# Kernel optimization log

Hardware: AMD Instinct MI355X
Metric: run time of the kernel (lower is better)

Reference implementation:

```python
import jax, jax.numpy as jnp
import numpy as np

EMBED_DIM = 512
NUM_HEADS = 8
HEAD_DIM = EMBED_DIM // NUM_HEADS
B, N, M = 4, 4096, 4096


def setup_inputs() -> dict:
    key = jax.random.key(0)
    ks = jax.random.split(key, 16)
    s = 0.02
    inp = {
        "query": jax.random.normal(ks[0], (B, N, EMBED_DIM), jnp.float32),
        "key": jax.random.normal(ks[1], (B, M, EMBED_DIM), jnp.float32),
        "value": jax.random.normal(ks[2], (B, M, EMBED_DIM), jnp.float32),
        # Linear weights stored as (in, out) so y = x @ W + b (== torch x @ W.T + b)
        "Wq": jax.random.normal(ks[3], (EMBED_DIM, EMBED_DIM), jnp.float32) * s,
        "bq": jnp.zeros((EMBED_DIM,), jnp.float32),
        "Wk": jax.random.normal(ks[4], (EMBED_DIM, EMBED_DIM), jnp.float32) * s,
        "bk": jnp.zeros((EMBED_DIM,), jnp.float32),
        "Wv": jax.random.normal(ks[5], (EMBED_DIM, EMBED_DIM), jnp.float32) * s,
        "bv": jnp.zeros((EMBED_DIM,), jnp.float32),
        # rank expansion MLP acts per-head on head_dim
        "W1": jax.random.normal(ks[6], (HEAD_DIM, HEAD_DIM * 2), jnp.float32) * s,
        "b1": jnp.zeros((HEAD_DIM * 2,), jnp.float32),
        "W2": jax.random.normal(ks[7], (HEAD_DIM * 2, HEAD_DIM), jnp.float32) * s,
        "b2": jnp.zeros((HEAD_DIM,), jnp.float32),
        "Wo": jax.random.normal(ks[8], (EMBED_DIM, EMBED_DIM), jnp.float32) * s,
        "bo": jnp.zeros((EMBED_DIM,), jnp.float32),
    }
    return inp


def reference(query, key, value, Wq, bq, Wk, bk, Wv, bv, W1, b1, W2, b2, Wo, bo):
    b, n, _ = query.shape
    m = key.shape[1]
    H, D = NUM_HEADS, HEAD_DIM
    # ELU+1 feature maps on projected q, k
    q = jax.nn.elu(query @ Wq + bq) + 1.0           # [B,N,E]
    k = jax.nn.elu(key @ Wk + bk) + 1.0             # [B,M,E]
    v = value @ Wv + bv                              # [B,M,E]
    q = q.reshape(b, n, H, D)
    k = k.reshape(b, m, H, D)
    v = v.reshape(b, m, H, D)
    # rank expansion MLP on keys (per head_dim), exact GELU as nn.GELU default
    k_aug = jax.nn.gelu(k @ W1 + b1, approximate=False) @ W2 + b2
    k_aug = jax.nn.elu(k_aug) + 1.0                  # [B,M,H,D]
    # inputs already fp32 (torch .float() casts are identity here)
    k_scaled = k_aug / m                             # normalize over context len
    kv_context = jnp.einsum('bmhd,bmhe->bhde', k_scaled, v)   # [B,H,D,D]
    out = jnp.einsum('bnhd,bhde->bnhe', q, kv_context)        # [B,N,H,D]
    k_sum = k_scaled.sum(axis=1)                      # [B,H,D]
    denom = jnp.einsum('bnhd,bhd->bnh', q, k_sum)     # [B,N,H]
    out = out / jnp.clip(denom, 1e-6, None)[..., None]
    out = jnp.clip(jnp.nan_to_num(out, nan=0.0, posinf=65000.0, neginf=-65000.0),
                   -65000.0, 65000.0)
    out = out.reshape(b, n, H * D)
    return out @ Wo + bo
```

## Files before the change

### kernel.cpp

```cpp
#include <hip/hip_runtime.h>
#include <hip/hip_bf16.h>
#include <cmath>

#define DEV __device__ __forceinline__

typedef __bf16 bf16x8 __attribute__((ext_vector_type(8)));
typedef float f32x4 __attribute__((ext_vector_type(4)));
typedef unsigned int u32;
typedef unsigned short u16;

#define S_VMCNT(N) asm volatile("s_waitcnt vmcnt(" #N ")" ::: "memory")
#define S_LGKM0    asm volatile("s_waitcnt lgkmcnt(0)" ::: "memory")
#define S_FENCE    asm volatile("" ::: "memory")
#define S_BAR      __builtin_amdgcn_s_barrier()

DEV u16 f2bf(float f) {
  union { float f; u32 u; } v;
  v.f = f;
  u32 u = v.u;
  u += 0x7fffu + ((u >> 16) & 1u);
  return (u16)(u >> 16);
}
DEV u32 pk2(float a, float b) {
  union { __hip_bfloat162 h2; u32 u; } v;
  v.h2 = __float22bfloat162_rn(float2{a, b});
  return v.u;
}

DEV void async16(const void* g, void* l) {
  __builtin_amdgcn_global_load_lds((const __attribute__((address_space(1))) u32*)g,
                                   (__attribute__((address_space(3))) u32*)l, 16, 0, 0);
}

DEV int swz(int row, int kq) { return row * 64 + ((kq * 8) ^ ((row & 7) << 3)); }

__global__ __launch_bounds__(256)
void prep_qkv(const float* __restrict__ qin, const float* __restrict__ kin,
              const float* __restrict__ vin, u16* __restrict__ qb,
              u16* __restrict__ kb, u16* __restrict__ vb)
{
  const int z = blockIdx.y;
  const float* src = z == 0 ? qin : z == 1 ? kin : vin;
  u16* dst = z == 0 ? qb : z == 1 ? kb : vb;
  const long r0 = (long)blockIdx.x * 64;
  const int tid = threadIdx.x;
#pragma unroll 4
  for (int it = 0; it < 16; ++it) {
    const int g = it * 256 + tid;
    const int rloc = g >> 6, kt = (g >> 3) & 7, kq = g & 7;
    const long ng = r0 + rloc;
    const int rb = (int)(ng >> 7), rl = (int)(ng & 127);
    const float* s = src + ng * 512 + kt * 64 + kq * 8;
    float4 lo = *(const float4*)s, hi = *(const float4*)(s + 4);
    union { u32 q[4]; uint4 v; } pk;
    pk.q[0] = pk2(lo.x, lo.y); pk.q[1] = pk2(lo.z, lo.w);
    pk.q[2] = pk2(hi.x, hi.y); pk.q[3] = pk2(hi.z, hi.w);
    *(uint4*)(dst + ((long)rb * 8 + kt) * 8192 + rl * 64 + ((kq * 8) ^ ((rl & 7) << 3))) = pk.v;
  }
}

__global__ __launch_bounds__(256, 2)
void qkv_gemm(const u16* __restrict__ qbI, const u16* __restrict__ kbI,
              const u16* __restrict__ vbI, const u16* __restrict__ WqP,
              const u16* __restrict__ WkP, const u16* __restrict__ WvP,
              const float* __restrict__ bq, const float* __restrict__ bk,
              const float* __restrict__ bv, const u16* __restrict__ W1T,
              const u16* __restrict__ W2T, const float* __restrict__ b1,
              const float* __restrict__ b2, u16* __restrict__ qact,
              u16* __restrict__ vT, u16* __restrict__ kaT, float invM)
{
  __shared__ __align__(16) u16 SB[32768];

  const int z = blockIdx.z;
  const u16* Ai = z == 0 ? qbI : z == 1 ? kbI : vbI;
  const u16* Bp = z == 0 ? WqP : z == 1 ? WkP : WvP;
  const float* bias = z == 0 ? bq : z == 1 ? bk : bv;

  const int tid = threadIdx.x, wv = tid >> 6, lane = tid & 63;
  const int wr = wv >> 1, wc = wv & 1;
  const int lrow = lane & 15, lq = lane >> 4;
  const long r0 = (long)blockIdx.x * 128;
  const int c0 = blockIdx.y * 128;

  auto stage = [&](int T, u16* buf) {
#pragma unroll
    for (int it = 0; it < 4; ++it) {
      const int sl = it * 256 + wv * 64;
      async16(Ai + ((long)blockIdx.x * 8 + T) * 8192 + (sl + lane) * 8, &buf[sl * 8]);
      async16(Bp + ((long)blockIdx.y * 8 + T) * 8192 + (sl + lane) * 8, &buf[8192 + sl * 8]);
    }
  };

  f32x4 acc[4][4] = {};
  stage(0, SB);
  S_VMCNT(0);
  S_BAR;

#pragma unroll
  for (int t = 0; t < 8; ++t) {
    const int cur = t & 1, nxt = 1 - cur;
    if (t < 7) stage(t + 1, SB + nxt * 16384);
    const u16* Ac = SB + cur * 16384;
    const u16* Bc = Ac + 8192;
#pragma unroll
    for (int subk = 0; subk < 2; ++subk) {
      bf16x8 af[4], bfr[4];
#pragma unroll
      for (int i = 0; i < 4; ++i)
        af[i] = *(const bf16x8*)&Ac[swz(wr * 64 + i * 16 + lrow, subk * 4 + lq)];
#pragma unroll
      for (int j = 0; j < 4; ++j)
        bfr[j] = *(const bf16x8*)&Bc[swz(wc * 64 + j * 16 + lrow, subk * 4 + lq)];
#pragma unroll
      for (int i = 0; i < 4; ++i)
#pragma unroll
        for (int j = 0; j < 4; ++j)
          acc[i][j] = __builtin_amdgcn_mfma_f32_16x16x32_bf16(af[i], bfr[j], acc[i][j], 0, 0, 0);
    }
    S_LGKM0;
    if (t < 7) { S_VMCNT(0); }
    S_BAR;
  }

  if (z == 0) {
#pragma unroll
    for (int i = 0; i < 4; ++i) {
#pragma unroll
      for (int j = 0; j < 4; ++j) {
        const int col = c0 + wc * 64 + j * 16 + lrow;
        const float bvv = bias[col];
#pragma unroll
        for (int p = 0; p < 4; ++p) {
          float o = acc[i][j][p] + bvv;
          o = (o > 0.f) ? (o + 1.f) : __expf(o);
          const long row = r0 + wr * 64 + i * 16 + lq * 4 + p;
          qact[row * 512 + col] = f2bf(o);
        }
      }
    }
  } else if (z == 2) {
    u16* LTv = SB + wv * 4608;
#pragma unroll
    for (int i = 0; i < 4; ++i) {
#pragma unroll
      for (int j = 0; j < 4; ++j) {
        const int col = c0 + wc * 64 + j * 16 + lrow;
        const float bvv = bias[col];
        ushort4 w;
        w.x = f2bf(acc[i][j][0] + bvv);
        w.y = f2bf(acc[i][j][1] + bvv);
        w.z = f2bf(acc[i][j][2] + bvv);
        w.w = f2bf(acc[i][j][3] + bvv);
        *(ushort4*)&LTv[(j * 16 + lrow) * 72 + i * 16 + lq * 4] = w;
      }
    }
    const int b = (int)(r0 >> 12);
    const int h = (c0 + wc * 64) >> 6;
    const int mg0 = (int)(r0 & 4095) + wr * 64;
    __syncthreads();
#pragma unroll
    for (int ps = 0; ps < 8; ++ps) {
      const int e = ps * 8 + (lane >> 3);
      const int mq = (lane & 7) * 8;
      uint4 v = *(const uint4*)&LTv[e * 72 + mq];
      *(uint4*)(vT + (((long)b * 8 + h) * 64 + e) * 4096 + mg0 + mq) = v;
    }
  } else {
    u16* As_k = SB;
    u16* hid  = SB + 16384;
    const int b   = (int)(r0 >> 12);
    const int m0g = (int)(r0 & 4095);
    const int h0  = c0 >> 6;

    __syncthreads();
#pragma unroll
    for (int i = 0; i < 4; ++i)
#pragma unroll
      for (int j = 0; j < 4; ++j) {
        const int col = c0 + wc * 64 + j * 16 + lrow;
        const float bvv = bias[col];
        const int d = j * 16 + lrow;
#pragma unroll
        for (int p = 0; p < 4; ++p) {
          const int m = wr * 64 + i * 16 + lq * 4 + p;
          float o = acc[i][j][p] + bvv;
          o = (o > 0.f) ? (o + 1.f) : __expf(o);
          As_k[wc * 8192 + m * 64 + ((((d >> 3) ^ (m & 7)) << 3) | (d & 7))] = f2bf(o);
        }
      }
    __syncthreads();

    const int c0m = (wv >> 1) * 64, mh0 = (wv & 1) * 64;
    const int d0  = (wv >> 1) * 32, mh2 = (wv & 1) * 64;

    for (int hh = 0; hh < 2; ++hh) {
      f32x4 acc1[4][4] = {};
#pragma unroll
      for (int kt = 0; kt < 2; ++kt) {
        bf16x8 wa[4], kb[4];
#pragma unroll
        for (int i = 0; i < 4; ++i)
          wa[i] = *(const bf16x8*)(W1T + (c0m + i * 16 + lrow) * 64 + kt * 32 + lq * 8);
#pragma unroll
        for (int j = 0; j < 4; ++j) {
          const int m = mh0 + j * 16 + lrow;
          kb[j] = *(const bf16x8*)&As_k[hh * 8192 + m * 64 + (((kt * 4 + lq) ^ (m & 7)) << 3)];
        }
#pragma unroll
        for (int i = 0; i < 4; ++i)
#pragma unroll
          for (int j = 0; j < 4; ++j)
            acc1[i][j] = __builtin_amdgcn_mfma_f32_16x16x32_bf16(wa[i], kb[j], acc1[i][j], 0, 0, 0);
      }

#pragma unroll
      for (int i = 0; i < 4; ++i) {
        const int cc = c0m + i * 16 + lq * 4;
        float4 bv4 = *(const float4*)(b1 + cc);
#pragma unroll
        for (int j = 0; j < 4; ++j) {
          const int m = mh0 + j * 16 + lrow;
          float x0 = acc1[i][j][0] + bv4.x, x1 = acc1[i][j][1] + bv4.y;
          float x2 = acc1[i][j][2] + bv4.z, x3 = acc1[i][j][3] + bv4.w;
          ushort4 w;
          w.x = f2bf(0.5f * x0 * (1.f + erff(x0 * 0.7071067811865475f)));
          w.y = f2bf(0.5f * x1 * (1.f + erff(x1 * 0.7071067811865475f)));
          w.z = f2bf(0.5f * x2 * (1.f + erff(x2 * 0.7071067811865475f)));
          w.w = f2bf(0.5f * x3 * (1.f + erff(x3 * 0.7071067811865475f)));
          *(ushort4*)&hid[m * 128 + ((((cc >> 3) ^ (m & 7)) << 3) | (cc & 7))] = w;
        }
      }
      __syncthreads();

      f32x4 acc2[4][2] = {};
#pragma unroll
      for (int kt = 0; kt < 4; ++kt) {
        bf16x8 wa2[2], hb[4];
#pragma unroll
        for (int i = 0; i < 2; ++i)
          wa2[i] = *(const bf16x8*)(W2T + (d0 + i * 16 + lrow) * 128 + kt * 32 + lq * 8);
#pragma unroll
        for (int j = 0; j < 4; ++j) {
          const int m = mh2 + j * 16 + lrow;
          hb[j] = *(const bf16x8*)&hid[m * 128 + (((kt * 4 + lq) ^ (m & 7)) << 3)];
        }
#pragma unroll
        for (int j = 0; j < 4; ++j)
#pragma unroll
          for (int i = 0; i < 2; ++i)
            acc2[j][i] = __builtin_amdgcn_mfma_f32_16x16x32_bf16(hb[j], wa2[i], acc2[j][i], 0, 0, 0);
      }

      u16* LT2 = SB + hh * 8192;
#pragma unroll
      for (int i = 0; i < 2; ++i) {
        const int d = d0 + i * 16 + lrow;
        const float bd = b2[d];
#pragma unroll
        for (int j = 0; j < 4; ++j) {
          const int ml = mh2 + j * 16 + lq * 4;
          ushort4 w;
#pragma unroll
          for (int p = 0; p < 4; ++p) {
            float v = acc2[j][i][p] + bd;
            v = ((v > 0.f) ? (v + 1.f) : __expf(v)) * invM;
            ((u16*)&w)[p] = f2bf(v);
          }
          *(ushort4*)&LT2[d * 128 + ((((ml >> 3) ^ (d & 7)) << 3) | (ml & 7))] = w;
        }
      }
      __syncthreads();

      const int bh2 = b * 8 + h0 + hh;
#pragma unroll
      for (int it = 0; it < 4; ++it) {
        const int u = it * 256 + tid;
        const int mo = u & 15, hd = u >> 4;
        uint4 v = *(const uint4*)&LT2[hd * 128 + ((mo ^ (hd & 7)) << 3)];
        *(uint4*)(kaT + ((long)bh2 * 64 + hd) * 4096 + m0g + mo * 8) = v;
      }
    }
  }
}

__global__ __launch_bounds__(256, 2)
void out_gemm(const u16* __restrict__ A, const u16* __restrict__ Bt,
              const float* __restrict__ bias, float* __restrict__ Y)
{
  __shared__ __align__(16) u16 SB[32768];
  const int tid = threadIdx.x, wv = tid >> 6, lane = tid & 63;
  const int wr = wv >> 1, wc = wv & 1;
  const int lrow = lane & 15, lq = lane >> 4;
  const long r0 = (long)blockIdx.x * 128;
  const int c0 = blockIdx.y * 128;

  auto stage = [&](int T, u16* buf) {
#pragma unroll
    for (int it = 0; it < 4; ++it) {
      const int sl = it * 256 + wv * 64;
      async16(A  + ((long)blockIdx.x * 8 + T) * 8192 + (sl + lane) * 8, &buf[sl * 8]);
      async16(Bt + ((long)blockIdx.y * 8 + T) * 8192 + (sl + lane) * 8, &buf[8192 + sl * 8]);
    }
  };

  f32x4 acc[4][4] = {};
  stage(0, SB);
  S_VMCNT(0);
  S_BAR;

#pragma unroll
  for (int t = 0; t < 8; ++t) {
    const int cur = t & 1, nxt = 1 - cur;
    if (t < 7) stage(t + 1, SB + nxt * 16384);
    const u16* Ac = SB + cur * 16384;
    const u16* Bc = Ac + 8192;
#pragma unroll
    for (int subk = 0; subk < 2; ++subk) {
      bf16x8 af[4], bfr[4];
#pragma unroll
      for (int i = 0; i < 4; ++i)
        af[i] = *(const bf16x8*)&Ac[swz(wr * 64 + i * 16 + lrow, subk * 4 + lq)];
#pragma unroll
      for (int j = 0; j < 4; ++j)
        bfr[j] = *(const bf16x8*)&Bc[swz(wc * 64 + j * 16 + lrow, subk * 4 + lq)];
#pragma unroll
      for (int i = 0; i < 4; ++i)
#pragma unroll
        for (int j = 0; j < 4; ++j)
          acc[i][j] = __builtin_amdgcn_mfma_f32_16x16x32_bf16(af[i], bfr[j], acc[i][j], 0, 0, 0);
    }
    S_LGKM0;
    if (t < 7) { S_VMCNT(0); }
    S_BAR;
  }
#pragma unroll
  for (int i = 0; i < 4; ++i) {
#pragma unroll
    for (int j = 0; j < 4; ++j) {
      const int col = c0 + wc * 64 + j * 16 + lrow;
      const float bv = bias[col];
#pragma unroll
      for (int p = 0; p < 4; ++p) {
        const long row = r0 + wr * 64 + i * 16 + lq * 4 + p;
        Y[row * 512 + col] = acc[i][j][p] + bv;
      }
    }
  }
}

struct TArgs {
  const float* src[6];
  u16* dst[6];
  int K[6];
  int N[6];
};
__global__ __launch_bounds__(256)
void transpose_w(TArgs a)
{
  const int m = blockIdx.z;
  const int K = a.K[m], N = a.N[m];
  const int kt = blockIdx.y * 64, nt = blockIdx.x * 64;
  if (kt >= K || nt >= N) return;
  const float* src = a.src[m];
  u16* dst = a.dst[m];
  __shared__ u16 t[64][72];
  const int tx = threadIdx.x & 15, ty = threadIdx.x >> 4;
#pragma unroll
  for (int rr = 0; rr < 64; rr += 16) {
    const int k = kt + ty + rr;
    float4 v = *(const float4*)(src + (long)k * N + nt + tx * 4);
    t[tx * 4 + 0][ty + rr] = f2bf(v.x);
    t[tx * 4 + 1][ty + rr] = f2bf(v.y);
    t[tx * 4 + 2][ty + rr] = f2bf(v.z);
    t[tx * 4 + 3][ty + rr] = f2bf(v.w);
  }
  __syncthreads();
  if (m < 4) {
    const int ktile = kt >> 6;
#pragma unroll
    for (int it = 0; it < 2; ++it) {
      const int s = threadIdx.x + it * 256;
      const int r = s >> 3, c = (s & 7) * 8;
      const int n = nt + r;
      const int colblk = n >> 7, cl = n & 127;
      ushort4 u0 = *(ushort4*)&t[r][c];
      ushort4 u1 = *(ushort4*)&t[r][c + 4];
      u16* d = dst + ((long)colblk * 8 + ktile) * 8192 + cl * 64 + (c ^ ((cl & 7) << 3));
      *(ushort4*)d = u0;
      *(ushort4*)(d + 4) = u1;
    }
  } else {
#pragma unroll
    for (int it = 0; it < 2; ++it) {
      const int s = threadIdx.x + it * 256;
      const int r = s >> 3, c = (s & 7) * 8;
      ushort4 u0 = *(ushort4*)&t[r][c];
      ushort4 u1 = *(ushort4*)&t[r][c + 4];
      *(ushort4*)(dst + (long)(nt + r) * K + kt + c) = u0;
      *(ushort4*)(dst + (long)(nt + r) * K + kt + c + 4) = u1;
    }
  }
}

__global__ __launch_bounds__(256, 2)
void kv_gemm(const u16* __restrict__ kaT, const u16* __restrict__ vT,
             float* __restrict__ kvp, float* __restrict__ ksp)
{
  const int sp = blockIdx.x;
  const int bh = blockIdx.y;
  __shared__ __align__(16) u16 SB[32768];
  const int tid = threadIdx.x, wv = tid >> 6, lane = tid & 63;
  const int lrow = lane & 15, lq = lane >> 4;
  f32x4 acc[4][4] = {};
  f32x4 accs[4] = {};
  bf16x8 ones;
#pragma unroll
  for (int z = 0; z < 8; ++z) ones[z] = (__bf16)1.0f;
  const long base = (long)bh * 64 * 4096;

#pragma unroll
  for (int ph = 0; ph < 2; ++ph) {
    const int m0 = sp * 256 + ph * 128;
#pragma unroll
    for (int i = 0; i < 4; ++i) {
      const int s = (wv * 4 + i) * 64 + lane;
      const int chunk = s >> 8, row = (s >> 2) & 63, part = s & 3;
      const long g = base + (long)row * 4096 + m0 + chunk * 32 + part * 8;
      async16(kaT + g, &SB[ph * 16384 + (wv * 4 + i) * 512]);
      async16(vT + g, &SB[ph * 16384 + 8192 + (wv * 4 + i) * 512]);
    }
    S_FENCE;
  }

#pragma unroll
  for (int ph = 0; ph < 2; ++ph) {
    if (ph == 0) { S_VMCNT(8); } else { S_VMCNT(0); }
    const u16* As = SB + ph * 16384;
    const u16* Bs = As + 8192;
    bf16x8 af[4], bfr[4];
#pragma unroll
    for (int i = 0; i < 4; ++i)
      af[i] = *(const bf16x8*)&As[wv * 2048 + (i * 16 + lrow) * 32 + lq * 8];
#pragma unroll
    for (int j = 0; j < 4; ++j)
      bfr[j] = *(const bf16x8*)&Bs[wv * 2048 + (j * 16 + lrow) * 32 + lq * 8];
#pragma unroll
    for (int i = 0; i < 4; ++i) {
#pragma unroll
      for (int j = 0; j < 4; ++j)
        acc[i][j] = __builtin_amdgcn_mfma_f32_16x16x32_bf16(af[i], bfr[j], acc[i][j], 0, 0, 0);
      accs[i] = __builtin_amdgcn_mfma_f32_16x16x32_bf16(af[i], ones, accs[i], 0, 0, 0);
    }
  }

  float* red = (float*)SB;
  float* ksr = red + 64 * 68;
  for (int w = 0; w < 4; ++w) {
    __syncthreads();
    if (wv == w) {
#pragma unroll
      for (int i = 0; i < 4; ++i) {
#pragma unroll
        for (int j = 0; j < 4; ++j) {
          const int e = j * 16 + lrow, dd = i * 16 + lq * 4;
          float* p = &red[e * 68 + dd];
          if (w == 0) { p[0] = acc[i][j][0]; p[1] = acc[i][j][1]; p[2] = acc[i][j][2]; p[3] = acc[i][j][3]; }
          else        { p[0] += acc[i][j][0]; p[1] += acc[i][j][1]; p[2] += acc[i][j][2]; p[3] += acc[i][j][3]; }
        }
        if (lrow == 0) {
          const int dd = i * 16 + lq * 4;
#pragma unroll
          for (int p2 = 0; p2 < 4; ++p2) {
            if (w == 0) ksr[dd + p2] = accs[i][p2];
            else        ksr[dd + p2] += accs[i][p2];
          }
        }
      }
    }
  }
  __syncthreads();
  float* kvo = kvp + ((long)sp * 32 + bh) * 4096;
  for (int s = tid; s < 4096; s += 256) kvo[s] = red[(s >> 6) * 68 + (s & 63)];
  if (tid < 64) ksp[(sp * 32 + bh) * 64 + tid] = ksr[tid];
}

__global__ __launch_bounds__(256)
void kv_reduce(const float* __restrict__ kvp, const float* __restrict__ ksp,
               u16* __restrict__ kvT, u16* __restrict__ ksumT)
{
  const int bh = blockIdx.x;
  const int t = threadIdx.x;
  const int s0 = blockIdx.y * 512;
#pragma unroll
  for (int i = 0; i < 2; ++i) {
    const int s = s0 + i * 256 + t;
    float v = 0.f;
#pragma unroll
    for (int sp = 0; sp < 16; ++sp) v += kvp[((long)sp * 32 + bh) * 4096 + s];
    kvT[(long)bh * 4096 + s] = f2bf(v);
  }
  if (blockIdx.y == 0 && t < 64) {
    float v = 0.f;
#pragma unroll
    for (int sp = 0; sp < 16; ++sp) v += ksp[(sp * 32 + bh) * 64 + t];
    ksumT[bh * 64 + t] = f2bf(v);
  }
}

__global__ __launch_bounds__(256)
void attn_mfma(const u16* __restrict__ q, const u16* __restrict__ kvT,
               const u16* __restrict__ ksumT, u16* __restrict__ attn)
{
  __shared__ u16 SB[17408];
  const int tid = threadIdx.x, wv = tid >> 6, lane = tid & 63;
  const int lrow = lane & 15, lq = lane >> 4;
  const int n0 = blockIdx.x * 256;
  const int bh = blockIdx.y, b = bh >> 3, h = bh & 7;
  u16* As = SB;

#pragma unroll
  for (int half = 0; half < 2; ++half)
#pragma unroll
    for (int i = 0; i < 4; ++i) {
      const int s = (wv * 4 + i) * 64 + lane;
      async16(q + ((long)(b * 4096 + n0 + (s >> 2))) * 512 + h * 64 + half * 32 + (s & 3) * 8,
              &As[half * 8192 + (wv * 4 + i) * 512]);
    }
  bf16x8 bfr[2][4], ks[2];
#pragma unroll
  for (int half = 0; half < 2; ++half) {
#pragma unroll
    for (int j = 0; j < 4; ++j)
      bfr[half][j] = *(const bf16x8*)(kvT + ((long)bh * 64 + j * 16 + lrow) * 64 + half * 32 + lq * 8);
    ks[half] = *(const bf16x8*)(ksumT + bh * 64 + half * 32 + lq * 8);
  }
  __syncthreads();

  f32x4 acc[4][4] = {};
  f32x4 accd[4] = {};
#pragma unroll
  for (int half = 0; half < 2; ++half) {
    bf16x8 af[4];
#pragma unroll
    for (int i = 0; i < 4; ++i)
      af[i] = *(const bf16x8*)&As[half * 8192 + (wv * 64 + i * 16 + lrow) * 32 + lq * 8];
#pragma unroll
    for (int i = 0; i < 4; ++i) {
#pragma unroll
      for (int j = 0; j < 4; ++j)
        acc[i][j] = __builtin_amdgcn_mfma_f32_16x16x32_bf16(af[i], bfr[half][j], acc[i][j], 0, 0, 0);
      accd[i] = __builtin_amdgcn_mfma_f32_16x16x32_bf16(af[i], ks[half], accd[i], 0, 0, 0);
    }
  }
  __syncthreads();

  u16* LT = SB;
#pragma unroll
  for (int i = 0; i < 4; ++i) {
    float dinv[4];
#pragma unroll
    for (int p = 0; p < 4; ++p) dinv[p] = 1.f / fmaxf(accd[i][p], 1e-6f);
#pragma unroll
    for (int j = 0; j < 4; ++j) {
      const int e = j * 16 + lrow;
      const int nl0 = i * 16 + lq * 4;
      ushort4 w;
      float x0 = acc[i][j][0] * dinv[0], x1 = acc[i][j][1] * dinv[1];
      float x2 = acc[i][j][2] * dinv[2], x3 = acc[i][j][3] * dinv[3];
      if (!(x0 == x0)) x0 = 0.f;
      if (!(x1 == x1)) x1 = 0.f;
      if (!(x2 == x2)) x2 = 0.f;
      if (!(x3 == x3)) x3 = 0.f;
      w.x = f2bf(fminf(65000.f, fmaxf(-65000.f, x0)));
      w.y = f2bf(fminf(65000.f, fmaxf(-65000.f, x1)));
      w.z = f2bf(fminf(65000.f, fmaxf(-65000.f, x2)));
      w.w = f2bf(fminf(65000.f, fmaxf(-65000.f, x3)));
      *(ushort4*)&LT[wv * 4352 + e * 68 + nl0] = w;
    }
  }
  __syncthreads();
#pragma unroll
  for (int it = 0; it < 8; ++it) {
    const int c = it * 256 + tid;
    const int n = c & 255, ec = c >> 8;
    const int wr2 = n >> 6, nl = n & 63;
    ushort4 w0, w1;
    w0.x = LT[wr2 * 4352 + (ec * 8 + 0) * 68 + nl];
    w0.y = LT[wr2 * 4352 + (ec * 8 + 1) * 68 + nl];
    w0.z = LT[wr2 * 4352 + (ec * 8 + 2) * 68 + nl];
    w0.w = LT[wr2 * 4352 + (ec * 8 + 3) * 68 + nl];
    w1.x = LT[wr2 * 4352 + (ec * 8 + 4) * 68 + nl];
    w1.y = LT[wr2 * 4352 + (ec * 8 + 5) * 68 + nl];
    w1.z = LT[wr2 * 4352 + (ec * 8 + 6) * 68 + nl];
    w1.w = LT[wr2 * 4352 + (ec * 8 + 7) * 68 + nl];
    const int ng = b * 4096 + n0 + n;
    const int rowblk = ng >> 7, rl = ng & 127;
    u16* dst = attn + ((long)rowblk * 8 + h) * 8192 + rl * 64 + ((ec * 8) ^ ((rl & 7) << 3));
    *(ushort4*)dst = w0;
    *(ushort4*)(dst + 4) = w1;
  }
}

static constexpr long U = 8388608;

extern "C" void kernel_launch(void* const* d_in, const int* in_sizes, int n_in,
                              void* d_out, int out_size, void* d_ws, size_t ws_size,
                              hipStream_t stream)
{
  const float* query = (const float*)d_in[0];
  const float* key   = (const float*)d_in[1];
  const float* value = (const float*)d_in[2];
  const float* Wq = (const float*)d_in[3];
  const float* bq = (const float*)d_in[4];
  const float* Wk = (const float*)d_in[5];
  const float* bk = (const float*)d_in[6];
  const float* Wv = (const float*)d_in[7];
  const float* bv = (const float*)d_in[8];
  const float* W1 = (const float*)d_in[9];
  const float* b1 = (const float*)d_in[10];
  const float* W2 = (const float*)d_in[11];
  const float* b2 = (const float*)d_in[12];
  const float* Wo = (const float*)d_in[13];
  const float* bo = (const float*)d_in[14];

  u16* wsh = (u16*)d_ws;
  u16* qact = wsh;
  u16* qb   = wsh + U;
  u16* vT   = wsh + 2 * U;
  u16* kaT  = wsh + 3 * U;
  u16* attn = wsh + 4 * U;
  u16* vb   = wsh + 4 * U;
  u16* kb   = (u16*)d_out;

  float* fp  = (float*)(wsh + 5 * U);
  float* kvp = fp;
  float* ksp = fp + 2097152;
  u16* kvTg   = (u16*)(fp + 2129920);
  u16* ksumTg = kvTg + 131072;
  u16* wtb = ksumTg + 2048;
  u16* WqT = wtb;
  u16* WkT = wtb + 262144;
  u16* WvT = wtb + 524288;
  u16* WoT = wtb + 786432;
  u16* W1T = wtb + 1048576;
  u16* W2T = wtb + 1056768;

  dim3 blk(256);
  const float invM = 1.f / 4096.f;

  TArgs ta;
  ta.src[0] = Wq; ta.dst[0] = WqT; ta.K[0] = 512; ta.N[0] = 512;
  ta.src[1] = Wk; ta.dst[1] = WkT; ta.K[1] = 512; ta.N[1] = 512;
  ta.src[2] = Wv; ta.dst[2] = WvT; ta.K[2] = 512; ta.N[2] = 512;
  ta.src[3] = Wo; ta.dst[3] = WoT; ta.K[3] = 512; ta.N[3] = 512;
  ta.src[4] = W1; ta.dst[4] = W1T; ta.K[4] = 64;  ta.N[4] = 128;
  ta.src[5] = W2; ta.dst[5] = W2T; ta.K[5] = 128; ta.N[5] = 64;
  transpose_w<<<dim3(8, 8, 6), blk, 0, stream>>>(ta);

  prep_qkv<<<dim3(256, 3), blk, 0, stream>>>(query, key, value, qb, kb, vb);

  qkv_gemm<<<dim3(128, 4, 3), blk, 0, stream>>>(qb, kb, vb, WqT, WkT, WvT,
                                                bq, bk, bv, W1T, W2T, b1, b2,
                                                qact, vT, kaT, invM);
  kv_gemm<<<dim3(16, 32), blk, 0, stream>>>(kaT, vT, kvp, ksp);
  kv_reduce<<<dim3(32, 8), blk, 0, stream>>>(kvp, ksp, kvTg, ksumTg);
  attn_mfma<<<dim3(16, 32), blk, 0, stream>>>(qact, kvTg, ksumTg, attn);
  out_gemm<<<dim3(128, 4), blk, 0, stream>>>(attn, WoT, bo, (float*)d_out);
}
```

Before: 264.4 us.

## Merge weight transpose into input prep kernel and stage q activation stores via LDS

```diff
diff --git a/kernel.cpp b/kernel.cpp
--- a/kernel.cpp
+++ b/kernel.cpp
@@ -34,28 +34,86 @@
 
 DEV int swz(int row, int kq) { return row * 64 + ((kq * 8) ^ ((row & 7) << 3)); }
 
+struct PArgs {
+  const float* wsrc[6];
+  u16* wdst[6];
+  int K[6];
+  int N[6];
+  const float* xsrc[3];
+  u16* xdst[3];
+};
 __global__ __launch_bounds__(256)
-void prep_qkv(const float* __restrict__ qin, const float* __restrict__ kin,
-              const float* __restrict__ vin, u16* __restrict__ qb,
-              u16* __restrict__ kb, u16* __restrict__ vb)
+void prep_all(PArgs a)
 {
-  const int z = blockIdx.y;
-  const float* src = z == 0 ? qin : z == 1 ? kin : vin;
-  u16* dst = z == 0 ? qb : z == 1 ? kb : vb;
-  const long r0 = (long)blockIdx.x * 64;
+  __shared__ u16 t[64][72];
   const int tid = threadIdx.x;
+
+  if (blockIdx.y == 3) {
+    const int x = blockIdx.x;
+    const int m = x >> 6;
+    const int kt = ((x >> 3) & 7) * 64, nt = (x & 7) * 64;
+    const int K = a.K[m], N = a.N[m];
+    if (kt >= K || nt >= N) return;
+    const float* src = a.wsrc[m];
+    u16* dst = a.wdst[m];
+    const int tx = tid & 15, ty = tid >> 4;
+#pragma unroll
+    for (int rr = 0; rr < 64; rr += 16) {
+      const int k = kt + ty + rr;
+      float4 v = *(const float4*)(src + (long)k * N + nt + tx * 4);
+      t[tx * 4 + 0][ty + rr] = f2bf(v.x);
+      t[tx * 4 + 1][ty + rr] = f2bf(v.y);
+      t[tx * 4 + 2][ty + rr] = f2bf(v.z);
+      t[tx * 4 + 3][ty + rr] = f2bf(v.w);
+    }
+    __syncthreads();
+    if (m < 4) {
+      const int ktile = kt >> 6;
+#pragma unroll
+      for (int it = 0; it < 2; ++it) {
+        const int s = tid + it * 256;
+        const int r = s >> 3, c = (s & 7) * 8;
+        const int n = nt + r;
+        const int colblk = n >> 7, cl = n & 127;
+        ushort4 u0 = *(ushort4*)&t[r][c];
+        ushort4 u1 = *(ushort4*)&t[r][c + 4];
+        u16* d = dst + ((long)colblk * 8 + ktile) * 8192 + cl * 64 + (c ^ ((cl & 7) << 3));
+        *(ushort4*)d = u0;
+        *(ushort4*)(d + 4) = u1;
+      }
+    } else {
+#pragma unroll
+      for (int it = 0; it < 2; ++it) {
+        const int s = tid + it * 256;
+        const int r = s >> 3, c = (s & 7) * 8;
+        ushort4 u0 = *(ushort4*)&t[r][c];
+        ushort4 u1 = *(ushort4*)&t[r][c + 4];
+        *(ushort4*)(dst + (long)(nt + r) * K + kt + c) = u0;
+        *(ushort4*)(dst + (long)(nt + r) * K + kt + c + 4) = u1;
+      }
+    }
+  } else {
+    if (blockIdx.x >= 256) return;
+    const int z = blockIdx.y;
+    const float* src = a.xsrc[z];
+    u16* dst = a.xdst[z];
+    const long r0 = (long)blockIdx.x * 64;
+    const int wv = tid >> 6, lane = tid & 63;
+    const int row_lo = lane >> 3, kq = lane & 7;
 #pragma unroll 4
-  for (int it = 0; it < 16; ++it) {
-    const int g = it * 256 + tid;
-    const int rloc = g >> 6, kt = (g >> 3) & 7, kq = g & 7;
-    const long ng = r0 + rloc;
-    const int rb = (int)(ng >> 7), rl = (int)(ng & 127);
-    const float* s = src + ng * 512 + kt * 64 + kq * 8;
-    float4 lo = *(const float4*)s, hi = *(const float4*)(s + 4);
-    union { u32 q[4]; uint4 v; } pk;
-    pk.q[0] = pk2(lo.x, lo.y); pk.q[1] = pk2(lo.z, lo.w);
-    pk.q[2] = pk2(hi.x, hi.y); pk.q[3] = pk2(hi.z, hi.w);
-    *(uint4*)(dst + ((long)rb * 8 + kt) * 8192 + rl * 64 + ((kq * 8) ^ ((rl & 7) << 3))) = pk.v;
+    for (int it = 0; it < 16; ++it) {
+      const int c = it * 4 + wv;
+      const int kt = c & 7, row_hi = c >> 3;
+      const int row = row_hi * 8 + row_lo;
+      const long ng = r0 + row;
+      const int rb = (int)(ng >> 7), rl = (int)(ng & 127);
+      const float* s = src + ng * 512 + kt * 64 + kq * 8;
+      float4 lo = *(const float4*)s, hi = *(const float4*)(s + 4);
+      union { u32 q[4]; uint4 v; } pk;
+      pk.q[0] = pk2(lo.x, lo.y); pk.q[1] = pk2(lo.z, lo.w);
+      pk.q[2] = pk2(hi.x, hi.y); pk.q[3] = pk2(hi.z, hi.w);
+      *(uint4*)(dst + ((long)rb * 8 + kt) * 8192 + rl * 64 + ((kq * 8) ^ ((rl & 7) << 3))) = pk.v;
+    }
   }
 }
 
@@ -123,20 +181,29 @@
   }
 
   if (z == 0) {
+    u16* LTq = SB + wv * 4608;
 #pragma unroll
     for (int i = 0; i < 4; ++i) {
 #pragma unroll
       for (int j = 0; j < 4; ++j) {
         const int col = c0 + wc * 64 + j * 16 + lrow;
         const float bvv = bias[col];
+        const int cloc = j * 16 + lrow;
 #pragma unroll
         for (int p = 0; p < 4; ++p) {
           float o = acc[i][j][p] + bvv;
           o = (o > 0.f) ? (o + 1.f) : __expf(o);
-          const long row = r0 + wr * 64 + i * 16 + lq * 4 + p;
-          qact[row * 512 + col] = f2bf(o);
-        }
-      }
+          LTq[(i * 16 + lq * 4 + p) * 72 + cloc] = f2bf(o);
+        }
+      }
+    }
+    __syncthreads();
+#pragma unroll
+    for (int ps = 0; ps < 8; ++ps) {
+      const int rloc = ps * 8 + (lane >> 3);
+      const int coff = (lane & 7) * 8;
+      uint4 v = *(const uint4*)&LTq[rloc * 72 + coff];
+      *(uint4*)(qact + (r0 + wr * 64 + rloc) * 512 + c0 + wc * 64 + coff) = v;
     }
   } else if (z == 2) {
     u16* LTv = SB + wv * 4608;
@@ -344,60 +411,6 @@
         const long row = r0 + wr * 64 + i * 16 + lq * 4 + p;
         Y[row * 512 + col] = acc[i][j][p] + bv;
       }
-    }
-  }
-}
-
-struct TArgs {
-  const float* src[6];
-  u16* dst[6];
-  int K[6];
-  int N[6];
-};
-__global__ __launch_bounds__(256)
-void transpose_w(TArgs a)
-{
-  const int m = blockIdx.z;
-  const int K = a.K[m], N = a.N[m];
-  const int kt = blockIdx.y * 64, nt = blockIdx.x * 64;
-  if (kt >= K || nt >= N) return;
-  const float* src = a.src[m];
-  u16* dst = a.dst[m];
-  __shared__ u16 t[64][72];
-  const int tx = threadIdx.x & 15, ty = threadIdx.x >> 4;
-#pragma unroll
-  for (int rr = 0; rr < 64; rr += 16) {
-    const int k = kt + ty + rr;
-    float4 v = *(const float4*)(src + (long)k * N + nt + tx * 4);
-    t[tx * 4 + 0][ty + rr] = f2bf(v.x);
-    t[tx * 4 + 1][ty + rr] = f2bf(v.y);
-    t[tx * 4 + 2][ty + rr] = f2bf(v.z);
-    t[tx * 4 + 3][ty + rr] = f2bf(v.w);
-  }
-  __syncthreads();
-  if (m < 4) {
-    const int ktile = kt >> 6;
-#pragma unroll
-    for (int it = 0; it < 2; ++it) {
-      const int s = threadIdx.x + it * 256;
-      const int r = s >> 3, c = (s & 7) * 8;
-      const int n = nt + r;
-      const int colblk = n >> 7, cl = n & 127;
-      ushort4 u0 = *(ushort4*)&t[r][c];
-      ushort4 u1 = *(ushort4*)&t[r][c + 4];
-      u16* d = dst + ((long)colblk * 8 + ktile) * 8192 + cl * 64 + (c ^ ((cl & 7) << 3));
-      *(ushort4*)d = u0;
-      *(ushort4*)(d + 4) = u1;
-    }
-  } else {
-#pragma unroll
-    for (int it = 0; it < 2; ++it) {
-      const int s = threadIdx.x + it * 256;
-      const int r = s >> 3, c = (s & 7) * 8;
-      ushort4 u0 = *(ushort4*)&t[r][c];
-      ushort4 u1 = *(ushort4*)&t[r][c + 4];
-      *(ushort4*)(dst + (long)(nt + r) * K + kt + c) = u0;
-      *(ushort4*)(dst + (long)(nt + r) * K + kt + c + 4) = u1;
     }
   }
 }
@@ -648,16 +661,17 @@
   dim3 blk(256);
   const float invM = 1.f / 4096.f;
 
-  TArgs ta;
-  ta.src[0] = Wq; ta.dst[0] = WqT; ta.K[0] = 512; ta.N[0] = 512;
-  ta.src[1] = Wk; ta.dst[1] = WkT; ta.K[1] = 512; ta.N[1] = 512;
-  ta.src[2] = Wv; ta.dst[2] = WvT; ta.K[2] = 512; ta.N[2] = 512;
-  ta.src[3] = Wo; ta.dst[3] = WoT; ta.K[3] = 512; ta.N[3] = 512;
-  ta.src[4] = W1; ta.dst[4] = W1T; ta.K[4] = 64;  ta.N[4] = 128;
-  ta.src[5] = W2; ta.dst[5] = W2T; ta.K[5] = 128; ta.N[5] = 64;
-  transpose_w<<<dim3(8, 8, 6), blk, 0, stream>>>(ta);
-
-  prep_qkv<<<dim3(256, 3), blk, 0, stream>>>(query, key, value, qb, kb, vb);
+  PArgs pa;
+  pa.wsrc[0] = Wq; pa.wdst[0] = WqT; pa.K[0] = 512; pa.N[0] = 512;
+  pa.wsrc[1] = Wk; pa.wdst[1] = WkT; pa.K[1] = 512; pa.N[1] = 512;
+  pa.wsrc[2] = Wv; pa.wdst[2] = WvT; pa.K[2] = 512; pa.N[2] = 512;
+  pa.wsrc[3] = Wo; pa.wdst[3] = WoT; pa.K[3] = 512; pa.N[3] = 512;
+  pa.wsrc[4] = W1; pa.wdst[4] = W1T; pa.K[4] = 64;  pa.N[4] = 128;
+  pa.wsrc[5] = W2; pa.wdst[5] = W2T; pa.K[5] = 128; pa.N[5] = 64;
+  pa.xsrc[0] = query; pa.xdst[0] = qb;
+  pa.xsrc[1] = key;   pa.xdst[1] = kb;
+  pa.xsrc[2] = value; pa.xdst[2] = vb;
+  prep_all<<<dim3(384, 4), blk, 0, stream>>>(pa);
 
   qkv_gemm<<<dim3(128, 4, 3), blk, 0, stream>>>(qb, kb, vb, WqT, WkT, WvT,
                                                 bq, bk, bv, W1T, W2T, b1, b2,
```

New measurement: 257.0 us. 1.03x faster.
